# Kernel optimization log

Hardware: AMD Instinct MI355X
Metric: run time of the kernel (lower is better)

Reference implementation:

```python
import jax, jax.numpy as jnp
import numpy as np

L = 10
DIL = tuple(2 ** i for i in range(L))  # dilations 1..512, kernel_size=2 -> one past tap, mem_size = dilation
DMAX = max(DIL)
R = 64            # residual channels
G = 2 * R         # gate channels (tanh | sigmoid)
S = 256           # skip channels
MEL = 80
NCLS = 256
HOP = 64
END = 256
FRAMES = 8


def setup_inputs() -> dict:
    ks = jax.random.split(jax.random.key(0), 16)
    sc = jnp.float32(0.1)
    n = lambda k, shape: jax.random.normal(k, shape, jnp.float32) * sc
    return {
        "y": jax.random.normal(ks[0], (MEL, FRAMES), jnp.float32),
        "samples": jax.random.uniform(ks[1], (FRAMES * HOP,), jnp.float32),
        "c": 1,
        "emb": jnp.tanh(n(ks[2], (NCLS, R))),               # buffer already tanh'ed in __init__
        "condition_W": n(ks[3], (L * G, MEL)),
        "WV_past_weight": n(ks[4], (L, G, R, 1)),            # kernel_size=2 -> 1 past tap
        "WV_present_weight": n(ks[5], (L, G, R)),
        "W_o_weight": n(ks[6], (L - 1, R + S, R)),
        "W_o_bias": n(ks[7], (L - 1, R + S)),
        "W_o_weight_last": n(ks[8], (S, R)),
        "W_o_bias_last": n(ks[9], (S,)),
        "end1_w": n(ks[10], (END, S)),
        "end1_b": n(ks[11], (END,)),
        "end2_w": n(ks[12], (NCLS, END)),
        "end2_b": n(ks[13], (NCLS,)),
    }


def _forward(y, samples, c, emb, condition_W, WV_past, WV_pres, W_o_w, W_o_b,
             W_o_wl, W_o_bl, e1w, e1b, e2w, e2b):
    # nearest-neighbor upsample of conditioning by hop_length (F.interpolate default mode)
    y_up = jnp.repeat(y, HOP, axis=1)                        # [MEL, T]
    T = y_up.shape[1]
    conds = (condition_W @ y_up).T.reshape(T, L, G)          # precompute all conditioning projections
    dil = jnp.array(DIL, jnp.int32)
    lidx = jnp.arange(L)

    def step(carry, xs):
        hist, prev = carry                                   # hist: [L, R, DMAX] shared ring buffer, global write ptr t%DMAX
        t, cond_t, s = xs
        x = emb[prev]                                        # [R]
        # value written dil[j] steps ago (zeros before warm-up), read before this step's write
        past = hist[lidx, :, (t - dil) % DMAX]               # [L, R]
        skip = jnp.zeros((S,), hist.dtype)
        written = []
        for j in range(L):
            h = cond_t[j] + WV_past[j, :, :, 0] @ past[j] + WV_pres[j] @ x
            zw, zf = jnp.split(h, 2)
            z = jnp.tanh(zw) * jax.nn.sigmoid(zf)
            written.append(x)                                # layer j stores its input in its ring buffer
            if j < L - 1:
                o = W_o_w[j] @ z + W_o_b[j]
                x = x + o[:R]
                skip = skip + o[R:]
            else:
                skip = skip + W_o_wl @ z + W_o_bl
        hist = hist.at[:, :, t % DMAX].set(jnp.stack(written))
        hid = jax.nn.relu(e1w @ jax.nn.relu(skip) + e1b)
        logits = (e2w @ hid + e2b) * c
        # inverse-CDF sampling: first index where cumsum(softmax) exceeds the uniform sample
        new = jnp.argmax(jnp.cumsum(jax.nn.softmax(logits)) > s).astype(jnp.int32)
        return (hist, new), (new, logits)

    carry0 = (jnp.zeros((L, R, DMAX), jnp.float32), jnp.int32(NCLS // 2 - 1))
    _, (outs, logits) = jax.lax.scan(step, carry0, (jnp.arange(T), conds, samples))
    return outs, logits


def reference(y, samples, c, emb, condition_W, WV_past_weight, WV_present_weight,
              W_o_weight, W_o_bias, W_o_weight_last, W_o_bias_last,
              end1_w, end1_b, end2_w, end2_b):
    outs, _ = _forward(y, samples, c, emb, condition_W, WV_past_weight,
                       WV_present_weight, W_o_weight, W_o_bias,
                       W_o_weight_last, W_o_bias_last, end1_w, end1_b, end2_w, end2_b)
    return outs
```

## Files before the change

### kernel.cpp

```cpp
#include <hip/hip_runtime.h>
#include <cmath>

#define L_     10
#define R_     64
#define G_     128
#define S_     256
#define MEL_   80
#define NCLS_  256
#define HOP_   64
#define END_   256
#define FRAMES_ 8
#define T_     512

typedef unsigned long long u64;

#define COND8_OFF   0
#define HIST_OFF    10240
#define MBX64_OFF   (HIST_OFF + 8*T_*R_)
#define CTR64_OFF   (MBX64_OFF + 4*R_*2)
#define HID64_OFF   (CTR64_OFF + 10*S_*2)
#define FLAG_OFF    (HID64_OFF + S_*2)

#define FID_PREV   11
#define FID_CLAIM  12

#define NROLE 7
#define SPIN_CAP (1 << 16)
#define LDS_SPIN_CAP (1 << 17)

__device__ __forceinline__ void push_tag(u64* p, float v, int tag) {
  u64 pk = ((u64)(unsigned)tag << 32) | (unsigned)__float_as_int(v);
  asm volatile("global_atomic_swap_x2 %0, %1, off" :: "v"(p), "v"(pk) : "memory");
}
__device__ __forceinline__ float poll_tag(u64* p, int want) {
  u64 r; int n = 0;
  do {
    asm volatile("global_atomic_add_x2 %0, %1, %2, off sc0\n\ts_waitcnt vmcnt(0)"
                 : "=&v"(r) : "v"(p), "v"(0ULL) : "memory");
    if ((int)(r >> 32) >= want) break;
  } while (++n <= SPIN_CAP);
  return __int_as_float((int)(unsigned)(r & 0xffffffffULL));
}
__device__ __forceinline__ float2 poll_tag2(u64* p0, u64* p1, int want) {
  u64 r0, r1; int n = 0;
  for (;;) {
    asm volatile("global_atomic_add_x2 %0, %2, %4, off sc0\n\t"
                 "global_atomic_add_x2 %1, %3, %4, off sc0\n\t"
                 "s_waitcnt vmcnt(0)"
                 : "=&v"(r0), "=&v"(r1) : "v"(p0), "v"(p1), "v"(0ULL) : "memory");
    if ((int)(r0 >> 32) >= want && (int)(r1 >> 32) >= want) break;
    if (++n > SPIN_CAP) break;
  }
  return make_float2(__int_as_float((int)(unsigned)(r0 & 0xffffffffULL)),
                     __int_as_float((int)(unsigned)(r1 & 0xffffffffULL)));
}
__device__ __forceinline__ int flag_poll_atomic(int* p) {
  int v;
  asm volatile("global_atomic_add %0, %1, %2, off sc0\n\ts_waitcnt vmcnt(0)"
               : "=&v"(v) : "v"(p), "v"(0) : "memory");
  return v;
}
__device__ __forceinline__ void push_flag(int* p, int v) {
  asm volatile("global_atomic_swap %0, %1, off" :: "v"(p), "v"(v) : "memory");
}
__device__ __forceinline__ int wait_prev_wave(int* p, int want, int lane) {
  int v = 0, n = 0;
  do {
    if (lane == 0) v = flag_poll_atomic(p);
    v = __shfl(v, 0, 64);
    if ((v >> 16) >= want) break;
  } while (++n <= SPIN_CAP);
  return v & 0xffff;
}

__device__ __forceinline__ void lds_spin_ge(int* p, int want) {
  int n = 0;
  while (__hip_atomic_load(p, __ATOMIC_ACQUIRE, __HIP_MEMORY_SCOPE_WORKGROUP) < want) {
    if (++n > LDS_SPIN_CAP) break;
  }
}
__device__ __forceinline__ void lds_store_rel(int* p, int v) {
  __hip_atomic_store(p, v, __ATOMIC_RELEASE, __HIP_MEMORY_SCOPE_WORKGROUP);
}
__device__ __forceinline__ void lds_add_rel(int* p) {
  (void)__hip_atomic_fetch_add(p, 1, __ATOMIC_RELEASE, __HIP_MEMORY_SCOPE_WORKGROUP);
}

#define DOTREG(N4, W, V4, ACC) do { \
  _Pragma("unroll") \
  for (int k_ = 0; k_ < (N4); ++k_) { float4 a_ = (V4)[k_]; \
    ACC = fmaf((W)[4*k_+0], a_.x, ACC); ACC = fmaf((W)[4*k_+1], a_.y, ACC); \
    ACC = fmaf((W)[4*k_+2], a_.z, ACC); ACC = fmaf((W)[4*k_+3], a_.w, ACC); } \
} while (0)

#define DOTREG_RELU(N4, W, V4, ACC) do { \
  _Pragma("unroll") \
  for (int k_ = 0; k_ < (N4); ++k_) { float4 a_ = (V4)[k_]; \
    a_.x = fmaxf(a_.x, 0.f); a_.y = fmaxf(a_.y, 0.f); \
    a_.z = fmaxf(a_.z, 0.f); a_.w = fmaxf(a_.w, 0.f); \
    ACC = fmaf((W)[4*k_+0], a_.x, ACC); ACC = fmaf((W)[4*k_+1], a_.y, ACC); \
    ACC = fmaf((W)[4*k_+2], a_.z, ACC); ACC = fmaf((W)[4*k_+3], a_.w, ACC); } \
} while (0)

__global__ void cond_prep_kernel(const float* __restrict__ condW,
                                 const float* __restrict__ y,
                                 float* __restrict__ cond8) {
  int idx = blockIdx.x * blockDim.x + threadIdx.x;
  if (idx >= FRAMES_ * L_ * G_) return;
  int f = idx / (L_ * G_);
  int row = idx - f * (L_ * G_);
  float acc = 0.f;
  for (int m = 0; m < MEL_; ++m)
    acc = fmaf(condW[row * MEL_ + m], y[m * FRAMES_ + f], acc);
  cond8[f * (L_ * G_) + row] = acc;
}

__global__ __launch_bounds__(256, 1) void wavenet_pipe(
    const float* __restrict__ samples,
    const int*   __restrict__ c_ptr,
    const float* __restrict__ emb,
    const float* __restrict__ WVp,
    const float* __restrict__ WVx,
    const float* __restrict__ Wo,
    const float* __restrict__ Wob,
    const float* __restrict__ Wol,
    const float* __restrict__ Wobl,
    const float* __restrict__ e1w,
    const float* __restrict__ e1b,
    const float* __restrict__ e2w,
    const float* __restrict__ e2b,
    float* __restrict__ ws,
    int*   __restrict__ out) {

  const int tid = threadIdx.x;

  float* cond8   = ws + COND8_OFF;
  float* hist    = ws + HIST_OFF;
  u64*   mbx     = (u64*)(ws + MBX64_OFF);
  u64*   contrib = (u64*)(ws + CTR64_OFF);
  u64*   mbhid   = (u64*)(ws + HID64_OFF);
  int*   flags   = (int*)(ws + FLAG_OFF);
  int*   fprev   = flags + FID_PREV * 16;

  __shared__ __align__(16) float x_s[R_];
  __shared__ __align__(16) float xb_s[R_];
  __shared__ __align__(16) float z_sa[R_];
  __shared__ __align__(16) float z_sb[R_];
  __shared__ __align__(16) float pd_sa[G_];
  __shared__ __align__(16) float pd_sb[G_];
  __shared__ __align__(16) float cond_a_s[FRAMES_ * G_];
  __shared__ __align__(16) float cond_b_s[FRAMES_ * G_];
  __shared__ __align__(16) float biasC_s[10 * S_];
  __shared__ __align__(16) float vec_s[S_];
  __shared__ float wred[4], wsum[4];
  __shared__ int wcand[4];
  __shared__ int role_s;
  __shared__ int zctr, cdone;

  {
    unsigned xcc;
    asm volatile("s_getreg_b32 %0, hwreg(HW_REG_XCC_ID)" : "=s"(xcc));
    if (tid == 0) {
      int r = -1;
      if (xcc == 0) {
        int c0 = atomicAdd(flags + FID_CLAIM * 16, 1);
        if (c0 < NROLE) r = c0;
      }
      role_s = r;
      zctr = 0; cdone = 0;
    }
    __syncthreads();
  }
  const int bid = role_s;
  if (bid < 0) return;

  if (bid < 5) {
    const int k = bid;
    const int j_a = 2 * k, j_b = 2 * k + 1;
    const int dil_a = 1 << j_a, dil_b = 1 << j_b;

    float* hist_a = (k > 0) ? (hist + (size_t)(j_a - 1) * T_ * R_) : nullptr;
    float* hist_b = (k < 4) ? (hist + (size_t)(j_b - 1) * T_ * R_) : nullptr;
    u64* mbx_in    = mbx + (size_t)(k - 1) * R_;
    u64* mbx_out   = mbx + (size_t)k * R_;
    u64* contrib_a = contrib + (size_t)j_a * S_;
    u64* contrib_b = contrib + (size_t)j_b * S_;

    for (int i = tid; i < FRAMES_ * G_; i += 256) {
      cond_a_s[i] = cond8[(i >> 7) * (L_ * G_) + j_a * G_ + (i & 127)];
      cond_b_s[i] = cond8[(i >> 7) * (L_ * G_) + j_b * G_ + (i & 127)];
    }

    if (tid < 64) {
      const int r = tid;
      float gw_a[64], gf_a[64], gw_b[64], gf_b[64], wres_a[64], wres_b[64];
      float ba0 = 0.f, bb0 = 0.f;
      {
        const float4* p;
        p = (const float4*)(WVx + ((size_t)(j_a * G_ + r)) * R_);
        #pragma unroll
        for (int i = 0; i < 16; ++i) ((float4*)gw_a)[i] = p[i];
        p = (const float4*)(WVx + ((size_t)(j_a * G_ + r + 64)) * R_);
        #pragma unroll
        for (int i = 0; i < 16; ++i) ((float4*)gf_a)[i] = p[i];
        p = (const float4*)(WVx + ((size_t)(j_b * G_ + r)) * R_);
        #pragma unroll
        for (int i = 0; i < 16; ++i) ((float4*)gw_b)[i] = p[i];
        p = (const float4*)(WVx + ((size_t)(j_b * G_ + r + 64)) * R_);
        #pragma unroll
        for (int i = 0; i < 16; ++i) ((float4*)gf_b)[i] = p[i];
        p = (const float4*)(Wo + ((size_t)(j_a * (R_ + S_) + r)) * R_);
        #pragma unroll
        for (int i = 0; i < 16; ++i) ((float4*)wres_a)[i] = p[i];
        ba0 = Wob[j_a * (R_ + S_) + r];
        if (k < 4) {
          p = (const float4*)(Wo + ((size_t)(j_b * (R_ + S_) + r)) * R_);
          #pragma unroll
          for (int i = 0; i < 16; ++i) ((float4*)wres_b)[i] = p[i];
          bb0 = Wob[j_b * (R_ + S_) + r];
        } else {
          p = (const float4*)(Wol + (size_t)r * R_);
          #pragma unroll
          for (int i = 0; i < 16; ++i) ((float4*)wres_b)[i] = p[i];
        }
      }
      __syncthreads();

      for (int t = 0; t < T_; ++t) {
        lds_spin_ge(&cdone, 3 * t);

        float x;
        if (k == 0) {
          int prev = 127;
          if (t > 0) prev = wait_prev_wave(fprev, t, r);
          x = emb[(size_t)prev * R_ + r];
        } else {
          x = poll_tag(mbx_in + r, t + 1);
        }
        x_s[r] = x;

        {
          const float4* x4 = (const float4*)x_s;
          float pdw = pd_sa[r], pdf = pd_sa[64 + r];
          float a0 = 0.f, a1 = 0.f, b0 = 0.f, b1 = 0.f;
          DOTREG(8, gw_a, x4, a0);       DOTREG(8, gw_a + 32, x4 + 8, a1);
          DOTREG(8, gf_a, x4, b0);       DOTREG(8, gf_a + 32, x4 + 8, b1);
          float hw = (a0 + a1) + pdw, hf = (b0 + b1) + pdf;
          z_sa[r] = tanhf(hw) * (1.f / (1.f + expf(-hf)));
        }
        if (r == 0) lds_store_rel(&zctr, 2 * t + 1);

        float xb;
        {
          float v0 = 0.f;
          DOTREG(16, wres_a, (const float4*)z_sa, v0);
          xb = x + v0 + ba0;
          xb_s[r] = xb;
        }

        {
          const float4* x4 = (const float4*)xb_s;
          float pdw = pd_sb[r], pdf = pd_sb[64 + r];
          float a0 = 0.f, a1 = 0.f, b0 = 0.f, b1 = 0.f;
          DOTREG(8, gw_b, x4, a0);       DOTREG(8, gw_b + 32, x4 + 8, a1);
          DOTREG(8, gf_b, x4, b0);       DOTREG(8, gf_b + 32, x4 + 8, b1);
          float hw = (a0 + a1) + pdw, hf = (b0 + b1) + pdf;
          z_sb[r] = tanhf(hw) * (1.f / (1.f + expf(-hf)));
        }
        if (r == 0) lds_store_rel(&zctr, 2 * t + 2);

        {
          float v0 = 0.f;
          DOTREG(16, wres_b, (const float4*)z_sb, v0);
          if (k < 4) push_tag(mbx_out + r, xb + v0 + bb0, t + 1);
          else       push_tag(contrib_b + r, v0, t + 1);
        }
      }

    } else {
      const int u = tid - 64;
      float wca1[64], wca2[64], wcb1[64], wcb2[64];
      {
        const float4* p;
        p = (const float4*)(Wo + ((size_t)(j_a * (R_ + S_) + 64 + u)) * R_);
        #pragma unroll
        for (int i = 0; i < 16; ++i) ((float4*)wca1)[i] = p[i];
        if (u < 64) {
          p = (const float4*)(Wo + ((size_t)(j_a * (R_ + S_) + 256 + u)) * R_);
          #pragma unroll
          for (int i = 0; i < 16; ++i) ((float4*)wca2)[i] = p[i];
        }
        if (k < 4) {
          p = (const float4*)(Wo + ((size_t)(j_b * (R_ + S_) + 64 + u)) * R_);
          #pragma unroll
          for (int i = 0; i < 16; ++i) ((float4*)wcb1)[i] = p[i];
          if (u < 64) {
            p = (const float4*)(Wo + ((size_t)(j_b * (R_ + S_) + 256 + u)) * R_);
            #pragma unroll
            for (int i = 0; i < 16; ++i) ((float4*)wcb2)[i] = p[i];
          }
        } else {
          p = (const float4*)(Wol + (size_t)(64 + u) * R_);
          #pragma unroll
          for (int i = 0; i < 16; ++i) ((float4*)wcb1)[i] = p[i];
        }
      }
      if (u >= 64) {
        const int pr = u - 64;
        pd_sa[pr] = cond_a_s[pr];
        pd_sb[pr] = cond_b_s[pr];
      }
      __syncthreads();

      for (int t = 0; t < T_; ++t) {
        lds_spin_ge(&zctr, 2 * t + 1);
        {
          float v = 0.f;
          DOTREG(16, wca1, (const float4*)z_sa, v);
          push_tag(contrib_a + u, v, t + 1);
          if (u < 64) {
            float v2 = 0.f;
            DOTREG(16, wca2, (const float4*)z_sa, v2);
            push_tag(contrib_a + 192 + u, v2, t + 1);
          }
        }
        if (k > 0 && u >= 176)
          ((float4*)(hist_a + (size_t)t * R_))[u - 176] = ((const float4*)x_s)[u - 176];

        lds_spin_ge(&zctr, 2 * t + 2);
        {
          float v = 0.f;
          DOTREG(16, wcb1, (const float4*)z_sb, v);
          push_tag(contrib_b + ((k < 4) ? u : (64 + u)), v, t + 1);
          if (k < 4 && u < 64) {
            float v2 = 0.f;
            DOTREG(16, wcb2, (const float4*)z_sb, v2);
            push_tag(contrib_b + 192 + u, v2, t + 1);
          }
        }
        if (k < 4 && u >= 160 && u < 176)
          ((float4*)(hist_b + (size_t)t * R_))[u - 160] = ((const float4*)xb_s)[u - 160];

        const int tn = t + 1;
        if (tn < T_ && u >= 64) {
          const int pr = u - 64;
          const int f1 = tn >> 6;
          float wtmp[64];
          {
            const float4* wp4 = (const float4*)(WVp + ((size_t)(j_a * G_ + pr)) * R_);
            #pragma unroll
            for (int i = 0; i < 16; ++i) ((float4*)wtmp)[i] = wp4[i];
            float a0 = 0.f, a1 = 0.f;
            if (k == 0) {
              const float4* p4 = (const float4*)x_s;
              DOTREG(8, wtmp, p4, a0);  DOTREG(8, wtmp + 32, p4 + 8, a1);
            } else {
              const int tp = tn - dil_a;
              if (tp >= 0) {
                const float4* p4 = (const float4*)(hist_a + (size_t)tp * R_);
                DOTREG(8, wtmp, p4, a0);  DOTREG(8, wtmp + 32, p4 + 8, a1);
              }
            }
            pd_sa[pr] = (a0 + a1) + cond_a_s[f1 * G_ + pr];
          }
          if (k < 4) {
            const float4* wp4 = (const float4*)(WVp + ((size_t)(j_b * G_ + pr)) * R_);
            #pragma unroll
            for (int i = 0; i < 16; ++i) ((float4*)wtmp)[i] = wp4[i];
            float a0 = 0.f, a1 = 0.f;
            const int tp = tn - dil_b;
            if (tp >= 0) {
              const float4* p4 = (const float4*)(hist_b + (size_t)tp * R_);
              DOTREG(8, wtmp, p4, a0);  DOTREG(8, wtmp + 32, p4 + 8, a1);
            }
            pd_sb[pr] = (a0 + a1) + cond_b_s[f1 * G_ + pr];
          } else {
            pd_sb[pr] = cond_b_s[f1 * G_ + pr];
          }
        }
        if ((u & 63) == 0) lds_add_rel(&cdone);
      }
    }

  } else if (bid == 5) {
    const int o_loc = tid >> 1, halfc = tid & 1;
    float w0[128], w1[128];
    {
      const float* p = e1w + ((size_t)o_loc) * S_ + halfc * 128;
      #pragma unroll
      for (int i = 0; i < 128; ++i) w0[i] = p[i];
      p = e1w + ((size_t)(128 + o_loc)) * S_ + halfc * 128;
      #pragma unroll
      for (int i = 0; i < 128; ++i) w1[i] = p[i];
    }
    const float bias0 = e1b[o_loc], bias1 = e1b[128 + o_loc];
    for (int i = tid; i < 10 * S_; i += 256) {
      int j = i >> 8, s = i & 255;
      biasC_s[i] = (j < 9) ? Wob[j * (R_ + S_) + 64 + s] : Wobl[s];
    }
    __syncthreads();

    for (int t = 0; t < T_; ++t) {
      float sacc = 0.f;
      for (int kk = 0; kk < 5; ++kk) {
        float2 v = poll_tag2(contrib + (size_t)(2 * kk) * S_ + tid,
                             contrib + (size_t)(2 * kk + 1) * S_ + tid, t + 1);
        sacc = (sacc + v.x) + biasC_s[(2 * kk) * S_ + tid];
        sacc = (sacc + v.y) + biasC_s[(2 * kk + 1) * S_ + tid];
      }
      vec_s[tid] = sacc;
      __syncthreads();
      const float4* s4 = (const float4*)(vec_s + halfc * 128);
      float v0 = 0.f, v1 = 0.f;
      DOTREG_RELU(32, w0, s4, v0);
      v0 += __shfl_down(v0, 1, 2);
      DOTREG_RELU(32, w1, s4, v1);
      v1 += __shfl_down(v1, 1, 2);
      if (halfc == 0) {
        push_tag(mbhid + o_loc,       fmaxf(v0 + bias0, 0.f), t + 1);
        push_tag(mbhid + 128 + o_loc, fmaxf(v1 + bias1, 0.f), t + 1);
      }
      __syncthreads();
    }

  } else {
    const int o_loc = tid >> 1, halfc = tid & 1;
    const float cf = (float)c_ptr[0];
    float w0[128], w1[128];
    {
      const float* p = e2w + ((size_t)o_loc) * END_ + halfc * 128;
      #pragma unroll
      for (int i = 0; i < 128; ++i) w0[i] = p[i];
      p = e2w + ((size_t)(128 + o_loc)) * END_ + halfc * 128;
      #pragma unroll
      for (int i = 0; i < 128; ++i) w1[i] = p[i];
    }
    const float bias0 = e2b[o_loc], bias1 = e2b[128 + o_loc];
    float* logits_s = cond_b_s;
    const int lane = tid & 63, wv = tid >> 6;

    for (int t = 0; t < T_; ++t) {
      vec_s[tid] = poll_tag(mbhid + tid, t + 1);
      __syncthreads();
      const float4* h4 = (const float4*)(vec_s + halfc * 128);
      float v0 = 0.f, v1 = 0.f;
      DOTREG(32, w0, h4, v0);
      v0 += __shfl_down(v0, 1, 2);
      DOTREG(32, w1, h4, v1);
      v1 += __shfl_down(v1, 1, 2);
      if (halfc == 0) {
        logits_s[o_loc]       = (v0 + bias0) * cf;
        logits_s[128 + o_loc] = (v1 + bias1) * cf;
      }
      __syncthreads();

      float lg = logits_s[tid];
      float m = lg;
      #pragma unroll
      for (int off = 32; off >= 1; off >>= 1) m = fmaxf(m, __shfl_xor(m, off, 64));
      if (lane == 0) wred[wv] = m;
      __syncthreads();
      m = fmaxf(fmaxf(wred[0], wred[1]), fmaxf(wred[2], wred[3]));
      float e = expf(lg - m);
      float cs = e;
      #pragma unroll
      for (int off = 1; off < 64; off <<= 1) {
        float o_ = __shfl_up(cs, off, 64);
        if (lane >= off) cs += o_;
      }
      if (lane == 63) wsum[wv] = cs;
      __syncthreads();
      float total = wsum[0] + wsum[1] + wsum[2] + wsum[3];
      float offv = 0.f;
      for (int w2 = 0; w2 < wv; ++w2) offv += wsum[w2];
      float thresh = samples[t] * total;
      bool flagb = (offv + cs) > thresh;
      unsigned long long mk = __ballot(flagb);
      if (lane == 0) wcand[wv] = mk ? (wv * 64 + __ffsll(mk) - 1) : 100000;
      __syncthreads();
      if (tid == 0) {
        int nw = min(min(wcand[0], wcand[1]), min(wcand[2], wcand[3]));
        if (nw >= 100000) nw = 0;
        out[t] = nw;
        push_flag(fprev, ((t + 1) << 16) | nw);
      }
      __syncthreads();
    }
  }
}

extern "C" void kernel_launch(void* const* d_in, const int* in_sizes, int n_in,
                              void* d_out, int out_size, void* d_ws, size_t ws_size,
                              hipStream_t stream) {
  const float* y       = (const float*)d_in[0];
  const float* samples = (const float*)d_in[1];
  const int*   c       = (const int*)d_in[2];
  const float* emb     = (const float*)d_in[3];
  const float* condW   = (const float*)d_in[4];
  const float* WVp     = (const float*)d_in[5];
  const float* WVx     = (const float*)d_in[6];
  const float* Wo      = (const float*)d_in[7];
  const float* Wob     = (const float*)d_in[8];
  const float* Wol     = (const float*)d_in[9];
  const float* Wobl    = (const float*)d_in[10];
  const float* e1w     = (const float*)d_in[11];
  const float* e1b     = (const float*)d_in[12];
  const float* e2w     = (const float*)d_in[13];
  const float* e2b     = (const float*)d_in[14];

  float* ws  = (float*)d_ws;
  int*   out = (int*)d_out;

  hipMemsetAsync((char*)d_ws + (size_t)FLAG_OFF * sizeof(float), 0,
                 16 * 16 * sizeof(int), stream);

  cond_prep_kernel<<<(FRAMES_ * L_ * G_ + 255) / 256, 256, 0, stream>>>(
      condW, y, ws + COND8_OFF);

  wavenet_pipe<<<256, 256, 0, stream>>>(samples, c, emb, WVp, WVx, Wo, Wob,
                                        Wol, Wobl, e1w, e1b, e2w, e2b, ws, out);
}
```

Measured before the change: 10.31 ms.

## Split layer-pair wavefront into separate waves per layer and stream skip weights

```diff
diff --git a/kernel.cpp b/kernel.cpp
--- a/kernel.cpp
+++ b/kernel.cpp
@@ -101,6 +101,26 @@
     ACC = fmaf((W)[4*k_+0], a_.x, ACC); ACC = fmaf((W)[4*k_+1], a_.y, ACC); \
     ACC = fmaf((W)[4*k_+2], a_.z, ACC); ACC = fmaf((W)[4*k_+3], a_.w, ACC); } \
 } while (0)
+
+__device__ __forceinline__ float dot64_stream(const float* wrow, const float* v_s) {
+  float w[64];
+  const float4* p = (const float4*)wrow;
+  #pragma unroll
+  for (int i = 0; i < 16; ++i) ((float4*)w)[i] = p[i];
+  float acc = 0.f;
+  DOTREG(16, w, (const float4*)v_s, acc);
+  return acc;
+}
+__device__ __forceinline__ float pddot_stream(const float* wrow, const float* v_s) {
+  float w[64];
+  const float4* p = (const float4*)wrow;
+  #pragma unroll
+  for (int i = 0; i < 16; ++i) ((float4*)w)[i] = p[i];
+  float a0 = 0.f, a1 = 0.f;
+  DOTREG(8, w, (const float4*)v_s, a0);
+  DOTREG(8, w + 32, ((const float4*)v_s) + 8, a1);
+  return a0 + a1;
+}
 
 __global__ void cond_prep_kernel(const float* __restrict__ condW,
                                  const float* __restrict__ y,
@@ -155,7 +175,7 @@
   __shared__ float wred[4], wsum[4];
   __shared__ int wcand[4];
   __shared__ int role_s;
-  __shared__ int zctr, cdone;
+  __shared__ int zctr, cdone, xbflag;
 
   {
     unsigned xcc;
@@ -167,7 +187,7 @@
         if (c0 < NROLE) r = c0;
       }
       role_s = r;
-      zctr = 0; cdone = 0;
+      zctr = 0; cdone = 0; xbflag = 0;
     }
     __syncthreads();
   }
@@ -190,11 +210,12 @@
       cond_a_s[i] = cond8[(i >> 7) * (L_ * G_) + j_a * G_ + (i & 127)];
       cond_b_s[i] = cond8[(i >> 7) * (L_ * G_) + j_b * G_ + (i & 127)];
     }
+    __syncthreads();
 
     if (tid < 64) {
       const int r = tid;
-      float gw_a[64], gf_a[64], gw_b[64], gf_b[64], wres_a[64], wres_b[64];
-      float ba0 = 0.f, bb0 = 0.f;
+      float gw_a[64], gf_a[64], wres_a[64];
+      float ba0;
       {
         const float4* p;
         p = (const float4*)(WVx + ((size_t)(j_a * G_ + r)) * R_);
@@ -203,16 +224,57 @@
         p = (const float4*)(WVx + ((size_t)(j_a * G_ + r + 64)) * R_);
         #pragma unroll
         for (int i = 0; i < 16; ++i) ((float4*)gf_a)[i] = p[i];
+        p = (const float4*)(Wo + ((size_t)(j_a * (R_ + S_) + r)) * R_);
+        #pragma unroll
+        for (int i = 0; i < 16; ++i) ((float4*)wres_a)[i] = p[i];
+        ba0 = Wob[j_a * (R_ + S_) + r];
+      }
+      __syncthreads();
+
+      for (int t = 0; t < T_; ++t) {
+        lds_spin_ge(&cdone, 2 * t);
+
+        float x;
+        if (k == 0) {
+          int prev = 127;
+          if (t > 0) prev = wait_prev_wave(fprev, t, r);
+          x = emb[(size_t)prev * R_ + r];
+        } else {
+          x = poll_tag(mbx_in + r, t + 1);
+        }
+        x_s[r] = x;
+
+        {
+          const float4* x4 = (const float4*)x_s;
+          float pdw = pd_sa[r], pdf = pd_sa[64 + r];
+          float a0 = 0.f, a1 = 0.f, b0 = 0.f, b1 = 0.f;
+          DOTREG(8, gw_a, x4, a0);       DOTREG(8, gw_a + 32, x4 + 8, a1);
+          DOTREG(8, gf_a, x4, b0);       DOTREG(8, gf_a + 32, x4 + 8, b1);
+          float hw = (a0 + a1) + pdw, hf = (b0 + b1) + pdf;
+          z_sa[r] = tanhf(hw) * (1.f / (1.f + expf(-hf)));
+        }
+        if (r == 0) lds_store_rel(&zctr, 2 * t + 1);
+
+        {
+          float v0 = 0.f;
+          DOTREG(16, wres_a, (const float4*)z_sa, v0);
+          xb_s[r] = x + v0 + ba0;
+        }
+        if (r == 0) lds_store_rel(&xbflag, t + 1);
+      }
+
+    } else if (tid < 128) {
+      const int r = tid - 64;
+      float gw_b[64], gf_b[64], wres_b[64];
+      float bb0 = 0.f;
+      {
+        const float4* p;
         p = (const float4*)(WVx + ((size_t)(j_b * G_ + r)) * R_);
         #pragma unroll
         for (int i = 0; i < 16; ++i) ((float4*)gw_b)[i] = p[i];
         p = (const float4*)(WVx + ((size_t)(j_b * G_ + r + 64)) * R_);
         #pragma unroll
         for (int i = 0; i < 16; ++i) ((float4*)gf_b)[i] = p[i];
-        p = (const float4*)(Wo + ((size_t)(j_a * (R_ + S_) + r)) * R_);
-        #pragma unroll
-        for (int i = 0; i < 16; ++i) ((float4*)wres_a)[i] = p[i];
-        ba0 = Wob[j_a * (R_ + S_) + r];
         if (k < 4) {
           p = (const float4*)(Wo + ((size_t)(j_b * (R_ + S_) + r)) * R_);
           #pragma unroll
@@ -227,36 +289,8 @@
       __syncthreads();
 
       for (int t = 0; t < T_; ++t) {
-        lds_spin_ge(&cdone, 3 * t);
-
-        float x;
-        if (k == 0) {
-          int prev = 127;
-          if (t > 0) prev = wait_prev_wave(fprev, t, r);
-          x = emb[(size_t)prev * R_ + r];
-        } else {
-          x = poll_tag(mbx_in + r, t + 1);
-        }
-        x_s[r] = x;
-
-        {
-          const float4* x4 = (const float4*)x_s;
-          float pdw = pd_sa[r], pdf = pd_sa[64 + r];
-          float a0 = 0.f, a1 = 0.f, b0 = 0.f, b1 = 0.f;
-          DOTREG(8, gw_a, x4, a0);       DOTREG(8, gw_a + 32, x4 + 8, a1);
-          DOTREG(8, gf_a, x4, b0);       DOTREG(8, gf_a + 32, x4 + 8, b1);
-          float hw = (a0 + a1) + pdw, hf = (b0 + b1) + pdf;
-          z_sa[r] = tanhf(hw) * (1.f / (1.f + expf(-hf)));
-        }
-        if (r == 0) lds_store_rel(&zctr, 2 * t + 1);
-
-        float xb;
-        {
-          float v0 = 0.f;
-          DOTREG(16, wres_a, (const float4*)z_sa, v0);
-          xb = x + v0 + ba0;
-          xb_s[r] = xb;
-        }
+        lds_spin_ge(&xbflag, t + 1);
+        float xb = xb_s[r];
 
         {
           const float4* x4 = (const float4*)xb_s;
@@ -278,104 +312,63 @@
       }
 
     } else {
-      const int u = tid - 64;
-      float wca1[64], wca2[64], wcb1[64], wcb2[64];
-      {
-        const float4* p;
-        p = (const float4*)(Wo + ((size_t)(j_a * (R_ + S_) + 64 + u)) * R_);
-        #pragma unroll
-        for (int i = 0; i < 16; ++i) ((float4*)wca1)[i] = p[i];
-        if (u < 64) {
-          p = (const float4*)(Wo + ((size_t)(j_a * (R_ + S_) + 256 + u)) * R_);
-          #pragma unroll
-          for (int i = 0; i < 16; ++i) ((float4*)wca2)[i] = p[i];
-        }
-        if (k < 4) {
-          p = (const float4*)(Wo + ((size_t)(j_b * (R_ + S_) + 64 + u)) * R_);
-          #pragma unroll
-          for (int i = 0; i < 16; ++i) ((float4*)wcb1)[i] = p[i];
-          if (u < 64) {
-            p = (const float4*)(Wo + ((size_t)(j_b * (R_ + S_) + 256 + u)) * R_);
-            #pragma unroll
-            for (int i = 0; i < 16; ++i) ((float4*)wcb2)[i] = p[i];
-          }
-        } else {
-          p = (const float4*)(Wol + (size_t)(64 + u) * R_);
-          #pragma unroll
-          for (int i = 0; i < 16; ++i) ((float4*)wcb1)[i] = p[i];
-        }
-      }
-      if (u >= 64) {
-        const int pr = u - 64;
-        pd_sa[pr] = cond_a_s[pr];
-        pd_sb[pr] = cond_b_s[pr];
-      }
+      const int u = tid - 128;
+      pd_sa[u] = cond_a_s[u];
+      pd_sb[u] = cond_b_s[u];
       __syncthreads();
 
       for (int t = 0; t < T_; ++t) {
         lds_spin_ge(&zctr, 2 * t + 1);
         {
-          float v = 0.f;
-          DOTREG(16, wca1, (const float4*)z_sa, v);
+          float v = dot64_stream(Wo + ((size_t)(j_a * (R_ + S_) + 64 + u)) * R_, z_sa);
           push_tag(contrib_a + u, v, t + 1);
+          float v2 = dot64_stream(Wo + ((size_t)(j_a * (R_ + S_) + 192 + u)) * R_, z_sa);
+          push_tag(contrib_a + 128 + u, v2, t + 1);
+        }
+        if (k > 0 && u >= 112)
+          ((float4*)(hist_a + (size_t)t * R_))[u - 112] = ((const float4*)x_s)[u - 112];
+
+        lds_spin_ge(&zctr, 2 * t + 2);
+        if (k < 4) {
+          float v = dot64_stream(Wo + ((size_t)(j_b * (R_ + S_) + 64 + u)) * R_, z_sb);
+          push_tag(contrib_b + u, v, t + 1);
+          float v2 = dot64_stream(Wo + ((size_t)(j_b * (R_ + S_) + 192 + u)) * R_, z_sb);
+          push_tag(contrib_b + 128 + u, v2, t + 1);
+        } else {
+          float v = dot64_stream(Wol + (size_t)(64 + u) * R_, z_sb);
+          push_tag(contrib_b + 64 + u, v, t + 1);
           if (u < 64) {
-            float v2 = 0.f;
-            DOTREG(16, wca2, (const float4*)z_sa, v2);
-            push_tag(contrib_a + 192 + u, v2, t + 1);
-          }
-        }
-        if (k > 0 && u >= 176)
-          ((float4*)(hist_a + (size_t)t * R_))[u - 176] = ((const float4*)x_s)[u - 176];
-
-        lds_spin_ge(&zctr, 2 * t + 2);
-        {
-          float v = 0.f;
-          DOTREG(16, wcb1, (const float4*)z_sb, v);
-          push_tag(contrib_b + ((k < 4) ? u : (64 + u)), v, t + 1);
-          if (k < 4 && u < 64) {
-            float v2 = 0.f;
-            DOTREG(16, wcb2, (const float4*)z_sb, v2);
+            float v2 = dot64_stream(Wol + (size_t)(192 + u) * R_, z_sb);
             push_tag(contrib_b + 192 + u, v2, t + 1);
           }
         }
-        if (k < 4 && u >= 160 && u < 176)
-          ((float4*)(hist_b + (size_t)t * R_))[u - 160] = ((const float4*)xb_s)[u - 160];
+        if (k < 4 && u >= 96 && u < 112)
+          ((float4*)(hist_b + (size_t)t * R_))[u - 96] = ((const float4*)xb_s)[u - 96];
 
         const int tn = t + 1;
-        if (tn < T_ && u >= 64) {
-          const int pr = u - 64;
+        if (tn < T_) {
           const int f1 = tn >> 6;
-          float wtmp[64];
           {
-            const float4* wp4 = (const float4*)(WVp + ((size_t)(j_a * G_ + pr)) * R_);
-            #pragma unroll
-            for (int i = 0; i < 16; ++i) ((float4*)wtmp)[i] = wp4[i];
-            float a0 = 0.f, a1 = 0.f;
+            float s = 0.f;
             if (k == 0) {
-              const float4* p4 = (const float4*)x_s;
-              DOTREG(8, wtmp, p4, a0);  DOTREG(8, wtmp + 32, p4 + 8, a1);
+              s = pddot_stream(WVp + ((size_t)(j_a * G_ + u)) * R_, x_s);
             } else {
               const int tp = tn - dil_a;
-              if (tp >= 0) {
-                const float4* p4 = (const float4*)(hist_a + (size_t)tp * R_);
-                DOTREG(8, wtmp, p4, a0);  DOTREG(8, wtmp + 32, p4 + 8, a1);
-              }
+              if (tp >= 0)
+                s = pddot_stream(WVp + ((size_t)(j_a * G_ + u)) * R_,
+                                 hist_a + (size_t)tp * R_);
             }
-            pd_sa[pr] = (a0 + a1) + cond_a_s[f1 * G_ + pr];
+            pd_sa[u] = s + cond_a_s[f1 * G_ + u];
           }
           if (k < 4) {
-            const float4* wp4 = (const float4*)(WVp + ((size_t)(j_b * G_ + pr)) * R_);
-            #pragma unroll
-            for (int i = 0; i < 16; ++i) ((float4*)wtmp)[i] = wp4[i];
-            float a0 = 0.f, a1 = 0.f;
+            float s = 0.f;
             const int tp = tn - dil_b;
-            if (tp >= 0) {
-              const float4* p4 = (const float4*)(hist_b + (size_t)tp * R_);
-              DOTREG(8, wtmp, p4, a0);  DOTREG(8, wtmp + 32, p4 + 8, a1);
-            }
-            pd_sb[pr] = (a0 + a1) + cond_b_s[f1 * G_ + pr];
+            if (tp >= 0)
+              s = pddot_stream(WVp + ((size_t)(j_b * G_ + u)) * R_,
+                               hist_b + (size_t)tp * R_);
+            pd_sb[u] = s + cond_b_s[f1 * G_ + u];
           } else {
-            pd_sb[pr] = cond_b_s[f1 * G_ + pr];
+            pd_sb[u] = cond_b_s[f1 * G_ + u];
           }
         }
         if ((u & 63) == 0) lds_add_rel(&cdone);
```

New measurement: 9.911 ms. 3.8% less time.
